# Kernel tuning notes

Hardware: AMD Instinct MI355X
Metric: run time of the kernel (lower is better)

The kernel has to match this reference:

```python
import jax, jax.numpy as jnp
import numpy as np

N, IN_CH, OUT_CH = 8192, 512, 512


def setup_inputs() -> dict:
    key = jax.random.key(0)
    ks = jax.random.split(key, 13)
    s = 1.0 / np.sqrt(IN_CH)
    return {
        "sp": jax.random.normal(ks[0], (N, IN_CH), jnp.float32),
        "om1": jax.random.normal(ks[1], (N, IN_CH), jnp.float32),
        "om2": jax.random.normal(ks[2], (N, IN_CH), jnp.float32),
        "q_w": jax.random.normal(ks[3], (OUT_CH, IN_CH), jnp.float32) * s,
        "q_b": jnp.zeros((OUT_CH,), jnp.float32),
        "k1_w": jax.random.normal(ks[4], (OUT_CH, IN_CH), jnp.float32) * s,
        "k1_b": jnp.zeros((OUT_CH,), jnp.float32),
        "k2_w": jax.random.normal(ks[5], (OUT_CH, IN_CH), jnp.float32) * s,
        "k2_b": jnp.zeros((OUT_CH,), jnp.float32),
        "v_w": jax.random.normal(ks[6], (OUT_CH, 3 * IN_CH), jnp.float32) * (1.0 / np.sqrt(3 * IN_CH)),
        "v_b": jnp.zeros((OUT_CH,), jnp.float32),
        "c1_w": jax.random.normal(ks[7], (OUT_CH, 2 * IN_CH), jnp.float32) * (1.0 / np.sqrt(2 * IN_CH)),
        "c1_b": jnp.zeros((OUT_CH,), jnp.float32),
    }


def reference(sp, om1, om2, q_w, q_b, k1_w, k1_b, k2_w, k2_b, v_w, v_b, c1_w, c1_b):
    # projections: nn.Linear -> x @ W.T + b
    q = sp @ q_w.T + q_b                                  # [N, out]
    k1 = om1 @ k1_w.T + k1_b                              # [N, out]
    k2 = om2 @ k2_w.T + k2_b                              # [N, out]
    om_cat = jnp.concatenate([sp, om1, om2], axis=-1)     # [N, 3*in]
    v = om_cat @ v_w.T + v_b                              # [N, out]

    scale = 1.0 / jnp.sqrt(jnp.asarray(q.shape[-1], q.dtype))
    attn1 = jax.nn.softmax(q @ k1.T * scale, axis=-1) @ v  # [N, out]
    attn2 = jax.nn.softmax(q @ k2.T * scale, axis=-1) @ v  # [N, out]

    # NOTE: source uses conf1's weights for BOTH gates (faithful to original)
    conf1 = jax.nn.sigmoid(jnp.concatenate([sp, om1], axis=-1) @ c1_w.T + c1_b)
    conf2 = jax.nn.sigmoid(jnp.concatenate([sp, om2], axis=-1) @ c1_w.T + c1_b)
    conf = jax.nn.softmax(jnp.stack([conf1, conf2], axis=-2), axis=-2)  # [N, 2, out]
    return conf[:, 0, :] * attn1 + conf[:, 1, :] * attn2
```

## Files before the change

kernel.cpp:

```cpp
#include <hip/hip_runtime.h>
#include <math.h>

typedef __bf16 bf16;
typedef __bf16 bf16x8 __attribute__((ext_vector_type(8)));
typedef float floatx4 __attribute__((ext_vector_type(4)));
typedef unsigned int u32;

#define MFMA16(a, b, c) __builtin_amdgcn_mfma_f32_16x16x32_bf16((a), (b), (c), 0, 0, 0)

static constexpr int NROWS = 8192;
static constexpr int DCH = 512;
static constexpr int QTILE = 64;
static constexpr int KTILE = 256;
static constexpr int NITER = NROWS / KTILE;
static constexpr float PRESCALE = 0.0637587130f;


__device__ __forceinline__ void async16(bf16* lds, const bf16* g) {
    __builtin_amdgcn_global_load_lds(
        (const __attribute__((address_space(1))) u32*)(const void*)g,
        (__attribute__((address_space(3))) u32*)(void*)lds, 16, 0, 0);
}

__device__ __forceinline__ void cvt_body(const float* __restrict__ in, bf16* __restrict__ out,
                                         int C, int i, float scale) {
    int c8 = i % (C >> 3);
    int r = i / (C >> 3);
    float4 v0 = ((const float4*)in)[i * 2];
    float4 v1 = ((const float4*)in)[i * 2 + 1];
    bf16x8 o;
    o[0] = (bf16)(v0.x * scale); o[1] = (bf16)(v0.y * scale);
    o[2] = (bf16)(v0.z * scale); o[3] = (bf16)(v0.w * scale);
    o[4] = (bf16)(v1.x * scale); o[5] = (bf16)(v1.y * scale);
    o[6] = (bf16)(v1.z * scale); o[7] = (bf16)(v1.w * scale);
    int nkb = C >> 5;
    size_t e = ((size_t)(r >> 4) * nkb + (c8 >> 2)) * 512 + (r & 15) * 32 + (c8 & 3) * 8;
    *(bf16x8*)(out + e) = o;
}

__global__ void cvt_blk_kernel(const float* __restrict__ in, bf16* __restrict__ out,
                               int C, int n8, float scale) {
    int i = blockIdx.x * blockDim.x + threadIdx.x;
    if (i >= n8) return;
    cvt_body(in, out, C, i, scale);
}

__global__ void cvt3_blk_kernel(const float* __restrict__ i0, const float* __restrict__ i1,
                                const float* __restrict__ i2,
                                bf16* __restrict__ o0, bf16* __restrict__ o1, bf16* __restrict__ o2,
                                int C, int n8, float s0, float s1, float s2) {
    int i = blockIdx.x * blockDim.x + threadIdx.x;
    if (i >= n8) return;
    const float* in;
    bf16* out;
    float sc;
    if (blockIdx.y == 0)      { in = i0; out = o0; sc = s0; }
    else if (blockIdx.y == 1) { in = i1; out = o1; sc = s1; }
    else                      { in = i2; out = o2; sc = s2; }
    cvt_body(in, out, C, i, sc);
}

__launch_bounds__(256, 4)
__global__ void proj_gemm(const bf16* __restrict__ spb, const bf16* __restrict__ om1b,
                          const bf16* __restrict__ om2b,
                          const bf16* __restrict__ qwb, const bf16* __restrict__ k1wb,
                          const bf16* __restrict__ k2wb, const bf16* __restrict__ vwb,
                          const bf16* __restrict__ c1wb,
                          const float* __restrict__ q_b, const float* __restrict__ k1_b,
                          const float* __restrict__ k2_b, const float* __restrict__ v_b,
                          const float* __restrict__ c1_b,
                          bf16* __restrict__ Q, bf16* __restrict__ K1, bf16* __restrict__ K2,
                          bf16* __restrict__ Vt, bf16* __restrict__ Z1, bf16* __restrict__ Z2) {
    __shared__ bf16 smA[16 * 512];
    __shared__ bf16 smB[16 * 512];

    const bf16* As[3] = {nullptr, nullptr, nullptr};
    int wofs[3] = {0, 0, 0};
    int nchunk = 1, ldw = 512, mode = 0;
    float bscale = 1.f;
    const bf16* W = nullptr;
    const float* bias = nullptr;
    bf16* out = nullptr;
    switch (blockIdx.z) {
        case 0: As[0] = spb;  W = qwb;  bias = q_b;  out = Q;  bscale = PRESCALE; break;
        case 1: As[0] = om1b; W = k1wb; bias = k1_b; out = K1; break;
        case 2: As[0] = om2b; W = k2wb; bias = k2_b; out = K2; break;
        case 3: As[0] = spb; As[1] = om1b; As[2] = om2b; nchunk = 3; W = vwb; ldw = 1536;
                wofs[1] = 512; wofs[2] = 1024; bias = v_b; out = Vt; mode = 1; break;
        case 4: As[0] = spb; As[1] = om1b; nchunk = 2; W = c1wb; ldw = 1024;
                wofs[1] = 512; bias = c1_b; out = Z1; mode = 2; break;
        default: As[0] = spb; As[1] = om2b; nchunk = 2; W = c1wb; ldw = 1024;
                wofs[1] = 512; bias = c1_b; out = Z2; mode = 2; break;
    }

    const int lane = threadIdx.x & 63;
    const int wv = threadIdx.x >> 6;
    const int m0 = blockIdx.y * 128 + (wv >> 1) * 64;
    const int n0 = blockIdx.x * 128 + (wv & 1) * 64;
    const int m0blk = blockIdx.y * 8;
    const int n0blk = blockIdx.x * 8;
    const int lm = lane & 15;
    const int r0 = (lane >> 4) * 4;
    const int nkbW = ldw >> 5;
    const int swz8 = (((lane >> 4) ^ ((lm >> 1) & 3))) * 8;
    const int lrow = lane >> 2;
    const int lsrc8 = ((lane & 3) ^ ((lane >> 3) & 3)) * 8;
    const int srw_m = (wv >> 1) * 4;
    const int srw_n = (wv & 1) * 4;

    floatx4 acc[4][4];
    #pragma unroll
    for (int mt = 0; mt < 4; ++mt)
        #pragma unroll
        for (int nt = 0; nt < 4; ++nt)
            acc[mt][nt] = (floatx4){0.f, 0.f, 0.f, 0.f};

    for (int c = 0; c < nchunk; ++c) {
        const bf16* __restrict__ A = As[c];
        const int wo = wofs[c];
        for (int kk = 0; kk < 512; kk += 64) {
            #pragma unroll
            for (int j = 0; j < 4; ++j) {
                int t = wv * 4 + j;
                int sr = t >> 1, kb = t & 1;
                const bf16* srcA = A + ((size_t)(m0blk + sr) * 16 + (kk >> 5) + kb) * 512
                                     + lrow * 32 + lsrc8;
                async16(smA + t * 512, srcA);
                const bf16* srcB = W + ((size_t)(n0blk + sr) * nkbW + ((wo + kk) >> 5) + kb) * 512
                                     + lrow * 32 + lsrc8;
                async16(smB + t * 512, srcB);
            }
            __syncthreads();
            #pragma unroll
            for (int kk2 = 0; kk2 < 2; ++kk2) {
                bf16x8 a[4], b[4];
                #pragma unroll
                for (int mt = 0; mt < 4; ++mt)
                    a[mt] = *(const bf16x8*)(smA + ((srw_m + mt) * 2 + kk2) * 512 + lm * 32 + swz8);
                #pragma unroll
                for (int nt = 0; nt < 4; ++nt)
                    b[nt] = *(const bf16x8*)(smB + ((srw_n + nt) * 2 + kk2) * 512 + lm * 32 + swz8);
                #pragma unroll
                for (int mt = 0; mt < 4; ++mt)
                    #pragma unroll
                    for (int nt = 0; nt < 4; ++nt)
                        acc[mt][nt] = MFMA16(a[mt], b[nt], acc[mt][nt]);
            }
            __syncthreads();
        }
    }

    #pragma unroll
    for (int mt = 0; mt < 4; ++mt)
        #pragma unroll
        for (int nt = 0; nt < 4; ++nt)
            #pragma unroll
            for (int i = 0; i < 4; ++i) {
                int m = m0 + mt * 16 + r0 + i;
                int n = n0 + nt * 16 + lm;
                float v = acc[mt][nt][i] + bias[n] * bscale;
                if (mode == 0)
                    out[((size_t)(m >> 4) * 16 + (n >> 5)) * 512 + (m & 15) * 32 + (n & 31)] = (bf16)v;
                else if (mode == 1)
                    out[((size_t)(n >> 4) * 256 + (m >> 5)) * 512 + (n & 15) * 32 + (m & 31)] = (bf16)v;
                else
                    out[(size_t)m * 512 + n] = (bf16)v;
            }
}

__launch_bounds__(1024, 4)
__global__ void attn_kernel(const bf16* __restrict__ Q, const bf16* __restrict__ K1g,
                            const bf16* __restrict__ K2g, const bf16* __restrict__ Vt,
                            bf16* __restrict__ On) {
    __shared__ bf16 Qs[64 * 512];
    __shared__ bf16 P[2 * 4 * 8 * 512];
    __shared__ float lsum[64];

    const int tid = threadIdx.x;
    const int lane = tid & 63;
    const int wv = tid >> 6;
    const int bid = blockIdx.x;
    const int att = bid & 1;
    const int q0 = (bid >> 1) * QTILE;
    const int lm = lane & 15;
    const int lk8 = (lane >> 4) * 8;
    const int r0 = (lane >> 4) * 4;
    const int ciq8 = ((lane >> 4) ^ ((lm >> 1) & 3)) * 8;

    {
        const bf16* Qg = Q + (size_t)(q0 >> 4) * (16 * 512);
        #pragma unroll
        for (int j = 0; j < 4; ++j) {
            int ch = tid + 1024 * j;
            bf16x8 v = *(const bf16x8*)(Qg + ch * 8);
            int r = (ch >> 2) & 15;
            int ci = ch & 3;
            int dst = (ch & ~3) * 8 + (ci ^ ((r >> 1) & 3)) * 8;
            *(bf16x8*)(Qs + dst) = v;
        }
    }
    if (tid < 64) lsum[tid] = 0.f;
    __syncthreads();

    const bf16* __restrict__ Kg = att ? K2g : K1g;
    const int d0 = wv * 32;

    floatx4 O[4][2];
    #pragma unroll
    for (int mt = 0; mt < 4; ++mt)
        #pragma unroll
        for (int nt = 0; nt < 2; ++nt)
            O[mt][nt] = (floatx4){0.f, 0.f, 0.f, 0.f};

    float lrs[4][4];
    #pragma unroll
    for (int mt = 0; mt < 4; ++mt)
        #pragma unroll
        for (int i = 0; i < 4; ++i) lrs[mt][i] = 0.f;

    auto phaseA = [&](int kt, int buf) {
        floatx4 s[4];
        #pragma unroll
        for (int mt = 0; mt < 4; ++mt) s[mt] = (floatx4){0.f, 0.f, 0.f, 0.f};
        const bf16* Kp = Kg + ((size_t)((kt >> 4) + wv) * 16) * 512 + lm * 32 + lk8;
        #pragma unroll
        for (int kb = 0; kb < 16; ++kb) {
            bf16x8 b = *(const bf16x8*)(Kp + kb * 512);
            #pragma unroll
            for (int mt = 0; mt < 4; ++mt) {
                bf16x8 a = *(const bf16x8*)(Qs + (mt * 16 + kb) * 512 + lm * 32 + ciq8);
                s[mt] = MFMA16(a, b, s[mt]);
            }
        }
        const int kb2 = wv >> 1;
        const int cb = (wv & 1) * 2;
        #pragma unroll
        for (int mt = 0; mt < 4; ++mt) {
            bf16* pt = P + (((buf * 4 + mt) * 8 + kb2) * 512);
            #pragma unroll
            for (int i = 0; i < 4; ++i) {
                float e = exp2f(s[mt][i]);
                int r = r0 + i;
                int ci = (cb + (lm >> 3)) ^ ((r >> 1) & 3);
                pt[r * 32 + ci * 8 + (lm & 7)] = (bf16)e;
                lrs[mt][i] += e;
            }
        }
    };

    auto phaseB = [&](int kt, int buf) {
        #pragma unroll
        for (int kk2 = 0; kk2 < 8; ++kk2) {
            bf16x8 p[4], bv[2];
            #pragma unroll
            for (int mt = 0; mt < 4; ++mt)
                p[mt] = *(const bf16x8*)(P + (((buf * 4 + mt) * 8 + kk2) * 512)
                                           + lm * 32 + ciq8);
            #pragma unroll
            for (int nt = 0; nt < 2; ++nt)
                bv[nt] = *(const bf16x8*)(Vt + ((size_t)((d0 >> 4) + nt) * 256 + (kt >> 5) + kk2) * 512
                                            + lm * 32 + lk8);
            #pragma unroll
            for (int mt = 0; mt < 4; ++mt)
                #pragma unroll
                for (int nt = 0; nt < 2; ++nt)
                    O[mt][nt] = MFMA16(p[mt], bv[nt], O[mt][nt]);
        }
    };

    phaseA(0, 0);
    __syncthreads();
    for (int it = 0; it < NITER; ++it) {
        int cur = it & 1;
        if (it + 1 < NITER) phaseA((it + 1) * KTILE, cur ^ 1);
        phaseB(it * KTILE, cur);
        __syncthreads();
    }

    #pragma unroll
    for (int mt = 0; mt < 4; ++mt)
        #pragma unroll
        for (int i = 0; i < 4; ++i) {
            float v = lrs[mt][i];
            v += __shfl_xor(v, 1); v += __shfl_xor(v, 2);
            v += __shfl_xor(v, 4); v += __shfl_xor(v, 8);
            if (lm == 0) atomicAdd(&lsum[mt * 16 + r0 + i], v);
        }
    __syncthreads();

    #pragma unroll
    for (int mt = 0; mt < 4; ++mt)
        #pragma unroll
        for (int nt = 0; nt < 2; ++nt)
            #pragma unroll
            for (int i = 0; i < 4; ++i) {
                int row = mt * 16 + r0 + i;
                int c = d0 + nt * 16 + lm;
                int c8s = ((c >> 3) ^ ((row >> 2) & 3)) * 8;
                Qs[row * 512 + c8s + (c & 7)] = (bf16)(O[mt][nt][i] / lsum[row]);
            }
    __syncthreads();
    {
        bf16* Op = On + (size_t)att * NROWS * 512 + (size_t)q0 * 512;
        #pragma unroll
        for (int j = 0; j < 4; ++j) {
            int ch = tid + 1024 * j;
            int r = ch >> 6;
            int c8 = ch & 63;
            *(bf16x8*)(Op + ch * 8) = *(const bf16x8*)(Qs + r * 512 + ((c8 ^ ((r >> 2) & 3)) * 8));
        }
    }
}

__global__ void gate_mix_kernel(const bf16* __restrict__ On, const bf16* __restrict__ Z1,
                                const bf16* __restrict__ Z2, float* __restrict__ out, int n4) {
    typedef __bf16 bf16x4v __attribute__((ext_vector_type(4)));
    int i = blockIdx.x * blockDim.x + threadIdx.x;
    if (i >= n4) return;
    const size_t NM = (size_t)NROWS * DCH;
    bf16x4v o1v = ((const bf16x4v*)On)[i];
    bf16x4v o2v = ((const bf16x4v*)(On + NM))[i];
    bf16x4v z1v = ((const bf16x4v*)Z1)[i];
    bf16x4v z2v = ((const bf16x4v*)Z2)[i];
    float4 r;
    float* rp = (float*)&r;
    #pragma unroll
    for (int j = 0; j < 4; ++j) {
        float g1 = 1.f / (1.f + __expf(-(float)z1v[j]));
        float g2 = 1.f / (1.f + __expf(-(float)z2v[j]));
        float w = 1.f / (1.f + __expf(-(g1 - g2)));
        rp[j] = w * (float)o1v[j] + (1.f - w) * (float)o2v[j];
    }
    ((float4*)out)[i] = r;
}

extern "C" void kernel_launch(void* const* d_in, const int* in_sizes, int n_in,
                              void* d_out, int out_size, void* d_ws, size_t ws_size,
                              hipStream_t stream) {
    const float* sp   = (const float*)d_in[0];
    const float* om1  = (const float*)d_in[1];
    const float* om2  = (const float*)d_in[2];
    const float* q_w  = (const float*)d_in[3];
    const float* q_b  = (const float*)d_in[4];
    const float* k1_w = (const float*)d_in[5];
    const float* k1_b = (const float*)d_in[6];
    const float* k2_w = (const float*)d_in[7];
    const float* k2_b = (const float*)d_in[8];
    const float* v_w  = (const float*)d_in[9];
    const float* v_b  = (const float*)d_in[10];
    const float* c1_w = (const float*)d_in[11];
    const float* c1_b = (const float*)d_in[12];
    float* out = (float*)d_out;

    char* ws = (char*)d_ws;
    size_t off = 0;
    auto alloc = [&](size_t bytes) -> void* {
        void* p = ws + off;
        off += (bytes + 255) & ~(size_t)255;
        return p;
    };
    const size_t NM = (size_t)NROWS * DCH;

    bf16* Q    = (bf16*)alloc(NM * 2);
    bf16* K1   = (bf16*)alloc(NM * 2);
    bf16* K2   = (bf16*)alloc(NM * 2);
    bf16* Vt   = (bf16*)alloc(NM * 2);
    bf16* Z1   = (bf16*)alloc(NM * 2);
    bf16* Z2   = (bf16*)alloc(NM * 2);
    bf16* On   = (bf16*)alloc((size_t)2 * NM * 2);

    bf16* spb  = (bf16*)alloc(NM * 2);
    bf16* om1b = (bf16*)alloc(NM * 2);
    bf16* om2b = (bf16*)alloc(NM * 2);
    bf16* qwb  = (bf16*)alloc(512 * 512 * 2);
    bf16* k1wb = (bf16*)alloc(512 * 512 * 2);
    bf16* k2wb = (bf16*)alloc(512 * 512 * 2);
    bf16* vwb  = (bf16*)alloc(512 * 1536 * 2);
    bf16* c1wb = (bf16*)alloc(512 * 1024 * 2);

    {
        int n8 = NROWS * 512 / 8;
        dim3 g((n8 + 255) / 256, 3);
        cvt3_blk_kernel<<<g, 256, 0, stream>>>(sp, om1, om2, spb, om1b, om2b, 512, n8,
                                               1.f, 1.f, 1.f);
    }
    {
        int n8 = 512 * 512 / 8;
        dim3 g((n8 + 255) / 256, 3);
        cvt3_blk_kernel<<<g, 256, 0, stream>>>(q_w, k1_w, k2_w, qwb, k1wb, k2wb, 512, n8,
                                               PRESCALE, 1.f, 1.f);
    }
    cvt_blk_kernel<<<(512 * 1536 / 8 + 255) / 256, 256, 0, stream>>>(v_w, vwb, 1536,
                                                                     512 * 1536 / 8, 1.f);
    cvt_blk_kernel<<<(512 * 1024 / 8 + 255) / 256, 256, 0, stream>>>(c1_w, c1wb, 1024,
                                                                     512 * 1024 / 8, 1.f);

    dim3 pgrid(512 / 128, NROWS / 128, 6);
    proj_gemm<<<pgrid, 256, 0, stream>>>(spb, om1b, om2b, qwb, k1wb, k2wb, vwb, c1wb,
                                         q_b, k1_b, k2_b, v_b, c1_b,
                                         Q, K1, K2, Vt, Z1, Z2);

    attn_kernel<<<(NROWS / QTILE) * 2, 1024, 0, stream>>>(Q, K1, K2, Vt, On);

    int n4 = (int)(NM / 4);
    gate_mix_kernel<<<(n4 + 255) / 256, 256, 0, stream>>>(On, Z1, Z2, out, n4);
}
```

Measured before the change: 529.2 us.

## Specialize warps into score-producer and PV-consumer groups in attention kernel

Splits the 16 waves into two roles: waves 0-7 compute QK^T scores and exponentials for the next key tile (two 16-key blocks each), while waves 8-15 do the P·V accumulation over 64 output columns each. Before, every wave did both phases. The aim is to overlap the score MFMAs with the PV MFMAs through the double-buffered P tile, a producer/consumer pipeline. The cost is more accumulator registers per wave (O grows to 4x4 and s to 4x2), which may lower occupancy or cause spills, and the two groups may be unevenly loaded.

```diff
diff --git a/kernel.cpp b/kernel.cpp
--- a/kernel.cpp
+++ b/kernel.cpp
@@ -203,13 +203,15 @@
     __syncthreads();
 
     const bf16* __restrict__ Kg = att ? K2g : K1g;
-    const int d0 = wv * 32;
-
-    floatx4 O[4][2];
+    const bool isA = wv < 8;
+    const int ks = wv & 7;
+    const int d0 = (wv & 7) * 64;
+
+    floatx4 O[4][4];
     #pragma unroll
     for (int mt = 0; mt < 4; ++mt)
         #pragma unroll
-        for (int nt = 0; nt < 2; ++nt)
+        for (int nt = 0; nt < 4; ++nt)
             O[mt][nt] = (floatx4){0.f, 0.f, 0.f, 0.f};
 
     float lrs[4][4];
@@ -219,86 +221,98 @@
         for (int i = 0; i < 4; ++i) lrs[mt][i] = 0.f;
 
     auto phaseA = [&](int kt, int buf) {
-        floatx4 s[4];
-        #pragma unroll
-        for (int mt = 0; mt < 4; ++mt) s[mt] = (floatx4){0.f, 0.f, 0.f, 0.f};
-        const bf16* Kp = Kg + ((size_t)((kt >> 4) + wv) * 16) * 512 + lm * 32 + lk8;
+        floatx4 s[4][2];
+        #pragma unroll
+        for (int mt = 0; mt < 4; ++mt) {
+            s[mt][0] = (floatx4){0.f, 0.f, 0.f, 0.f};
+            s[mt][1] = (floatx4){0.f, 0.f, 0.f, 0.f};
+        }
+        const bf16* Kp = Kg + ((size_t)((kt >> 4) + ks * 2) * 16) * 512 + lm * 32 + lk8;
         #pragma unroll
         for (int kb = 0; kb < 16; ++kb) {
-            bf16x8 b = *(const bf16x8*)(Kp + kb * 512);
+            bf16x8 b0 = *(const bf16x8*)(Kp + kb * 512);
+            bf16x8 b1 = *(const bf16x8*)(Kp + 16 * 512 + kb * 512);
             #pragma unroll
             for (int mt = 0; mt < 4; ++mt) {
                 bf16x8 a = *(const bf16x8*)(Qs + (mt * 16 + kb) * 512 + lm * 32 + ciq8);
-                s[mt] = MFMA16(a, b, s[mt]);
+                s[mt][0] = MFMA16(a, b0, s[mt][0]);
+                s[mt][1] = MFMA16(a, b1, s[mt][1]);
             }
         }
-        const int kb2 = wv >> 1;
-        const int cb = (wv & 1) * 2;
         #pragma unroll
         for (int mt = 0; mt < 4; ++mt) {
-            bf16* pt = P + (((buf * 4 + mt) * 8 + kb2) * 512);
-            #pragma unroll
-            for (int i = 0; i < 4; ++i) {
-                float e = exp2f(s[mt][i]);
-                int r = r0 + i;
-                int ci = (cb + (lm >> 3)) ^ ((r >> 1) & 3);
-                pt[r * 32 + ci * 8 + (lm & 7)] = (bf16)e;
-                lrs[mt][i] += e;
-            }
+            bf16* pt = P + (((buf * 4 + mt) * 8 + ks) * 512);
+            #pragma unroll
+            for (int kf = 0; kf < 2; ++kf)
+                #pragma unroll
+                for (int i = 0; i < 4; ++i) {
+                    float e = exp2f(s[mt][kf][i]);
+                    int r = r0 + i;
+                    int ci = (kf * 2 + (lm >> 3)) ^ ((r >> 1) & 3);
+                    pt[r * 32 + ci * 8 + (lm & 7)] = (bf16)e;
+                    lrs[mt][i] += e;
+                }
         }
     };
 
     auto phaseB = [&](int kt, int buf) {
         #pragma unroll
         for (int kk2 = 0; kk2 < 8; ++kk2) {
-            bf16x8 p[4], bv[2];
+            bf16x8 p[4], bv[4];
             #pragma unroll
             for (int mt = 0; mt < 4; ++mt)
                 p[mt] = *(const bf16x8*)(P + (((buf * 4 + mt) * 8 + kk2) * 512)
                                            + lm * 32 + ciq8);
             #pragma unroll
-            for (int nt = 0; nt < 2; ++nt)
+            for (int nt = 0; nt < 4; ++nt)
                 bv[nt] = *(const bf16x8*)(Vt + ((size_t)((d0 >> 4) + nt) * 256 + (kt >> 5) + kk2) * 512
                                             + lm * 32 + lk8);
             #pragma unroll
             for (int mt = 0; mt < 4; ++mt)
                 #pragma unroll
-                for (int nt = 0; nt < 2; ++nt)
+                for (int nt = 0; nt < 4; ++nt)
                     O[mt][nt] = MFMA16(p[mt], bv[nt], O[mt][nt]);
         }
     };
 
-    phaseA(0, 0);
+    if (isA) phaseA(0, 0);
     __syncthreads();
     for (int it = 0; it < NITER; ++it) {
         int cur = it & 1;
-        if (it + 1 < NITER) phaseA((it + 1) * KTILE, cur ^ 1);
-        phaseB(it * KTILE, cur);
+        if (isA) {
+            if (it + 1 < NITER) phaseA((it + 1) * KTILE, cur ^ 1);
+        } else {
+            phaseB(it * KTILE, cur);
+        }
         __syncthreads();
     }
 
-    #pragma unroll
-    for (int mt = 0; mt < 4; ++mt)
-        #pragma unroll
-        for (int i = 0; i < 4; ++i) {
-            float v = lrs[mt][i];
-            v += __shfl_xor(v, 1); v += __shfl_xor(v, 2);
-            v += __shfl_xor(v, 4); v += __shfl_xor(v, 8);
-            if (lm == 0) atomicAdd(&lsum[mt * 16 + r0 + i], v);
-        }
+    if (isA) {
+        #pragma unroll
+        for (int mt = 0; mt < 4; ++mt)
+            #pragma unroll
+            for (int i = 0; i < 4; ++i) {
+                float v = lrs[mt][i];
+                v += __shfl_xor(v, 1); v += __shfl_xor(v, 2);
+                v += __shfl_xor(v, 4); v += __shfl_xor(v, 8);
+                if (lm == 0) atomicAdd(&lsum[mt * 16 + r0 + i], v);
+            }
+    }
     __syncthreads();
 
-    #pragma unroll
-    for (int mt = 0; mt < 4; ++mt)
-        #pragma unroll
-        for (int nt = 0; nt < 2; ++nt)
-            #pragma unroll
-            for (int i = 0; i < 4; ++i) {
-                int row = mt * 16 + r0 + i;
-                int c = d0 + nt * 16 + lm;
-                int c8s = ((c >> 3) ^ ((row >> 2) & 3)) * 8;
-                Qs[row * 512 + c8s + (c & 7)] = (bf16)(O[mt][nt][i] / lsum[row]);
-            }
+    if (!isA) {
+        #pragma unroll
+        for (int mt = 0; mt < 4; ++mt)
+            #pragma unroll
+            for (int nt = 0; nt < 4; ++nt)
+                #pragma unroll
+                for (int i = 0; i < 4; ++i) {
+                    int row = mt * 16 + r0 + i;
+                    int c = d0 + nt * 16 + lm;
+                    int c8s = ((c >> 3) ^ ((row >> 2) & 3)) * 8;
+                    Qs[row * 512 + c8s + (c & 7)] = (bf16)(O[mt][nt][i] / lsum[row]);
+                }
+    }
     __syncthreads();
     {
         bf16* Op = On + (size_t)att * NROWS * 512 + (size_t)q0 * 512;
```

New measurement: 624.7 us. +18.0%, slower.
